# Kernel tuning notes

Hardware: AMD Instinct MI355X
Metric: run time of the kernel (lower is better)

The kernel has to match this reference:

```python
import jax, jax.numpy as jnp
import numpy as np

HEADS, DQK, DV = 4, 128, 128
HH, WW = 32, 32
SCALE = DQK ** -0.5
EPS = 1e-5


def bn(x, g, b, m, v):
    # eval-mode BatchNorm2d over channel dim of NCHW
    inv = g * jax.lax.rsqrt(v + EPS)
    return x * inv[:, None, None] + (b - m * inv)[:, None, None]


def rel_to_abs(x):
    # x: (B, Nh, L, 2L-1) -> (B, Nh, L, L)
    B, Nh, L, _ = x.shape
    x = jnp.pad(x, ((0, 0), (0, 0), (0, 0), (0, 1)))
    fx = x.reshape(B, Nh, L * 2 * L)
    fx = jnp.pad(fx, ((0, 0), (0, 0), (0, L - 1)))
    fx = fx.reshape(B, Nh, L + 1, 2 * L - 1)
    return fx[:, :, :L, L - 1:]


def rel_logits_1d(q, rel_k):
    # q: (B, Nh, H, W, D); rel_k: (2W-1, D)
    B, Nh, H, W, D = q.shape
    r = jnp.einsum('bnhwd,rd->bnhwr', q, rel_k)
    r = rel_to_abs(r.reshape(B, Nh * H, W, 2 * W - 1))
    r = r.reshape(B, Nh, H, W, W)
    return jnp.broadcast_to(r[:, :, :, None], (B, Nh, H, H, W, W))


def pos_bias(q, rel_h, rel_w):
    # q: (B, Nh, H*W, D), already scaled
    B, Nh, L, D = q.shape
    q5 = q.reshape(B, Nh, HH, WW, D)
    rw = rel_logits_1d(q5, rel_w)                     # (B,N,H,Hx,W,W)
    rw = rw.transpose(0, 1, 2, 4, 3, 5).reshape(B, Nh, HH * WW, HH * WW)
    rh = rel_logits_1d(q5.transpose(0, 1, 3, 2, 4), rel_h)  # (B,N,W,Wx,H,H)
    rh = rh.transpose(0, 1, 4, 2, 5, 3).reshape(B, Nh, HH * WW, HH * WW)
    return rw + rh


def to_heads(x):
    # (B, Nh*d, H, W) -> (B, Nh, H*W, d)
    B, C, H, W = x.shape
    x = x.reshape(B, HEADS, C // HEADS, H, W)
    return x.transpose(0, 1, 3, 4, 2).reshape(B, HEADS, H * W, C // HEADS)


def mhsa(x, w_qk, w_v, rel_h, rel_w):
    B, C, H, W = x.shape
    qk = jnp.einsum('bchw,oc->bohw', x, w_qk)
    q, k = jnp.split(qk, 2, axis=1)
    v = jnp.einsum('bchw,oc->bohw', x, w_v)
    q, k, v = to_heads(q), to_heads(k), to_heads(v)
    q = q * SCALE
    logits = jnp.einsum('bnid,bnjd->bnij', q, k) + pos_bias(q, rel_h, rel_w)
    weights = jax.nn.softmax(logits, axis=-1)
    out = jnp.einsum('bnij,bnjd->bnid', weights, v)   # (B,Nh,HW,dv)
    out = out.reshape(B, HEADS, H, W, DV).transpose(0, 1, 4, 2, 3)
    return out.reshape(B, HEADS * DV, H, W)


def setup_inputs() -> dict:
    key = jax.random.key(0)
    ks = jax.random.split(key, 12)
    d = {
        'x': jax.random.normal(ks[0], (8, 512, HH, WW), jnp.float32),
        'w_qk': jax.random.normal(ks[1], (2 * HEADS * DQK, 512), jnp.float32) * 0.02,
        'w_v': jax.random.normal(ks[2], (HEADS * DV, 512), jnp.float32) * 0.02,
        'rel_h': jax.random.normal(ks[3], (2 * HH - 1, DQK), jnp.float32) * SCALE,
        'rel_w': jax.random.normal(ks[4], (2 * WW - 1, DQK), jnp.float32) * SCALE,
        'g1': jnp.ones((512,), jnp.float32),
        'b1': jnp.zeros((512,), jnp.float32),
        'm1': jax.random.normal(ks[5], (512,), jnp.float32) * 0.1,
        'v1': jax.random.uniform(ks[6], (512,), jnp.float32) + 0.5,
        'g2': jnp.ones((512,), jnp.float32),
        'b2': jnp.zeros((512,), jnp.float32),
        'm2': jax.random.normal(ks[7], (512,), jnp.float32) * 0.1,
        'v2': jax.random.uniform(ks[8], (512,), jnp.float32) + 0.5,
        'w_fc': jax.random.normal(ks[9], (512, 512, 3, 3), jnp.float32) * 0.02,
        'bias_fc': jnp.zeros((512,), jnp.float32),
    }
    return d


def reference(x, w_qk, w_v, rel_h, rel_w, g1, b1, m1, v1, g2, b2, m2, v2, w_fc, bias_fc):
    out = jax.nn.relu(bn(x, g1, b1, m1, v1))
    out = mhsa(out, w_qk, w_v, rel_h, rel_w)
    x = out + x
    out = jax.nn.relu(bn(x, g2, b2, m2, v2))
    out = jax.lax.conv_general_dilated(
        out, w_fc, window_strides=(1, 1), padding='SAME',
        dimension_numbers=('NCHW', 'OIHW', 'NCHW')) + bias_fc[:, None, None]
    return out + x
```

## Files before the change

### kernel.cpp

```cpp
#include <hip/hip_runtime.h>

typedef __bf16 v8bf __attribute__((ext_vector_type(8)));
typedef float f32x4 __attribute__((ext_vector_type(4)));

#define DEVI static __device__ __forceinline__

DEVI v8bf load8(const __bf16* p) { return *reinterpret_cast<const v8bf*>(p); }

DEVI f32x4 mfma16(v8bf a, v8bf b, f32x4 c) {
  return __builtin_amdgcn_mfma_f32_16x16x32_bf16(a, b, c, 0, 0, 0);
}

DEVI void gld16(const __bf16* g, __bf16* l) {
  __builtin_amdgcn_global_load_lds(
      (const __attribute__((address_space(1))) unsigned int*)(const void*)g,
      (__attribute__((address_space(3))) unsigned int*)(void*)l, 16, 0, 0);
}

#define SCALE_Q 0.08838834764831845f

__global__ void k_prep(const float* __restrict__ wqk, const float* __restrict__ wv,
                       const float* __restrict__ relh, const float* __restrict__ relw,
                       const float* __restrict__ wfc, __bf16* __restrict__ wqkb,
                       __bf16* __restrict__ wvb, __bf16* __restrict__ rhb,
                       __bf16* __restrict__ rwb, __bf16* __restrict__ Wt,
                       float* __restrict__ zpad4, const float* __restrict__ x,
                       const float* __restrict__ g1, const float* __restrict__ b1,
                       const float* __restrict__ m1, const float* __restrict__ v1,
                       __bf16* __restrict__ y) {
  __shared__ float tile[32][33];
  const int bid = blockIdx.x, tid = threadIdx.x;
  if (bid >= 6472) {
    const int local = bid - 6472;
    const int b = local >> 9, c0 = ((local >> 5) & 15) * 32, s0 = (local & 31) * 32;
    const int tx = tid & 31, ty = tid >> 5;
#pragma unroll
    for (int r = 0; r < 4; ++r) {
      int c = c0 + ty + r * 8;
      float inv = g1[c] * rsqrtf(v1[c] + 1e-5f);
      float beta = b1[c] - m1[c] * inv;
      float val = x[((size_t)b * 512 + c) * 1024 + s0 + tx] * inv + beta;
      tile[ty + r * 8][tx] = fmaxf(val, 0.0f);
    }
    __syncthreads();
#pragma unroll
    for (int r = 0; r < 4; ++r) {
      int s = s0 + ty + r * 8;
      y[((size_t)b * 1024 + s) * 512 + c0 + tx] = (__bf16)tile[tx][ty + r * 8];
    }
    return;
  }
  if (bid < 2048) {
    int i = bid * 256 + tid;
    wqkb[i] = (__bf16)wqk[i];
  } else if (bid < 3072) {
    int i = (bid - 2048) * 256 + tid;
    wvb[i] = (__bf16)wv[i];
  } else if (bid < 3104) {
    int i = (bid - 3072) * 256 + tid;
    if (i < 8064) rhb[i] = (__bf16)relh[i];
  } else if (bid < 3136) {
    int i = (bid - 3104) * 256 + tid;
    if (i < 8064) rwb[i] = (__bf16)relw[i];
  } else if (bid < 4160) {
    int i = (bid - 3136) * 256 + tid;
    const float* src = wfc + (size_t)i * 9;
#pragma unroll
    for (int tap = 0; tap < 9; ++tap)
      Wt[(size_t)tap * 262144 + i] = (__bf16)src[tap];
  } else {
    int i = (bid - 4160) * 256 + tid;
    f32x4 z = {0.f, 0.f, 0.f, 0.f};
    reinterpret_cast<f32x4*>(zpad4)[i] = z;
  }
}

__global__ void k_bn2c(float* o0x2, const float* __restrict__ o1,
                       const float* __restrict__ lp, const float* __restrict__ xin,
                       const float* __restrict__ g, const float* __restrict__ bb,
                       const float* __restrict__ m, const float* __restrict__ v,
                       __bf16* __restrict__ zp) {
  __shared__ float tile[32][33];
  const int b = blockIdx.z, c0 = blockIdx.y * 32, s0 = blockIdx.x * 32;
  const int tx = threadIdx.x, ty = threadIdx.y;
  const int bnrow = b * 4 + (c0 >> 7);
  const int scol = s0 + tx;
  const float linv =
      1.0f / (lp[bnrow * 1024 + scol] + lp[32768 + bnrow * 1024 + scol]);
#pragma unroll
  for (int r = 0; r < 4; ++r) {
    int c = c0 + ty + r * 8;
    float inv = g[c] * rsqrtf(v[c] + 1e-5f);
    float beta = bb[c] - m[c] * inv;
    size_t idx = ((size_t)b * 512 + c) * 1024 + scol;
    float t = (o0x2[idx] + o1[idx]) * linv + xin[idx];
    o0x2[idx] = t;
    tile[ty + r * 8][tx] = fmaxf(t * inv + beta, 0.0f);
  }
  __syncthreads();
#pragma unroll
  for (int r = 0; r < 4; ++r) {
    int s = s0 + ty + r * 8;
    int hh = s >> 5, ww = s & 31;
    zp[(((size_t)b * 34 + hh + 1) * 34 + ww + 1) * 512 + c0 + tx] =
        (__bf16)tile[tx][ty + r * 8];
  }
}

__global__ __launch_bounds__(256) void k_proj(
    const __bf16* __restrict__ wall, const __bf16* __restrict__ y,
    __bf16* __restrict__ qout, __bf16* __restrict__ kout,
    __bf16* __restrict__ vout) {
  __shared__ __bf16 As[2][128 * 32];
  __shared__ __bf16 Bs[2][128 * 32];
  const int t = threadIdx.x;
  const int wave = t >> 6, lane = t & 63;
  const int l15 = lane & 15, quad = lane >> 4;
  const int Lb = blockIdx.x;
  const int logical = (Lb & 7) * 96 + (Lb >> 3);
  const int nt = logical / 12, mt = logical % 12;
  const int mbase = mt * 128;
  const int nbase = nt * 128;
  const int mh = (wave >> 1) * 64, nh = (wave & 1) * 64;
  const bool isv = mbase >= 1024;

  const int row0 = t >> 2, part8 = (t & 3) * 8;
  const __bf16* gA0 = wall + (size_t)(mbase + row0) * 512 + part8;
  const __bf16* gA1 = gA0 + (size_t)64 * 512;
  const __bf16* gB0 = y + (size_t)(nbase + row0) * 512 + part8;
  const __bf16* gB1 = gB0 + (size_t)64 * 512;
  const int wofs = wave * 512;

  const f32x4 fz = {0.f, 0.f, 0.f, 0.f};
  f32x4 acc[4][4];
#pragma unroll
  for (int i = 0; i < 4; ++i)
#pragma unroll
    for (int j = 0; j < 4; ++j) acc[i][j] = fz;

  gld16(gA0, &As[0][wofs]);
  gld16(gA1, &As[0][2048 + wofs]);
  gld16(gB0, &Bs[0][wofs]);
  gld16(gB1, &Bs[0][2048 + wofs]);
  __syncthreads();

#pragma unroll 1
  for (int r = 0; r < 16; ++r) {
    const int cur = r & 1;
    if (r < 15) {
      const int kn = (r + 1) * 32;
      gld16(gA0 + kn, &As[cur ^ 1][wofs]);
      gld16(gA1 + kn, &As[cur ^ 1][2048 + wofs]);
      gld16(gB0 + kn, &Bs[cur ^ 1][wofs]);
      gld16(gB1 + kn, &Bs[cur ^ 1][2048 + wofs]);
    }
    v8bf a[4], bfr[4];
#pragma unroll
    for (int i = 0; i < 4; ++i)
      a[i] = load8(&As[cur][(mh + i * 16 + l15) * 32 + quad * 8]);
#pragma unroll
    for (int j = 0; j < 4; ++j)
      bfr[j] = load8(&Bs[cur][(nh + j * 16 + l15) * 32 + quad * 8]);
    if (isv) {
#pragma unroll
      for (int i = 0; i < 4; ++i)
#pragma unroll
        for (int j = 0; j < 4; ++j) acc[i][j] = mfma16(a[i], bfr[j], acc[i][j]);
    } else {
#pragma unroll
      for (int i = 0; i < 4; ++i)
#pragma unroll
        for (int j = 0; j < 4; ++j) acc[i][j] = mfma16(bfr[j], a[i], acc[i][j]);
    }
    __syncthreads();
  }

  if (isv) {
#pragma unroll
    for (int i = 0; i < 4; ++i)
#pragma unroll
      for (int j = 0; j < 4; ++j)
#pragma unroll
        for (int r = 0; r < 4; ++r) {
          int o = mbase + mh + i * 16 + quad * 4 + r;
          int nflat = nbase + nh + j * 16 + l15;
          int b = nflat >> 10, s = nflat & 1023;
          int oe = o - 1024; int n = oe >> 7, d = oe & 127;
          vout[(((size_t)b * 4 + n) * 128 + d) * 1024 + s] = (__bf16)acc[i][j][r];
        }
  } else {
    const bool isq = mbase < 512;
#pragma unroll
    for (int i = 0; i < 4; ++i)
#pragma unroll
      for (int j = 0; j < 4; ++j)
#pragma unroll
        for (int r = 0; r < 4; ++r) {
          int o = mbase + mh + i * 16 + l15;
          int nflat = nbase + nh + j * 16 + quad * 4 + r;
          int b = nflat >> 10, s = nflat & 1023;
          float val = acc[i][j][r];
          if (isq) {
            int n = o >> 7, d = o & 127;
            qout[(((size_t)b * 4 + n) * 1024 + s) * 128 + d] = (__bf16)(val * SCALE_Q);
          } else {
            int oe = o - 512; int n = oe >> 7, d = oe & 127;
            kout[(((size_t)b * 4 + n) * 1024 + s) * 128 + d] = (__bf16)val;
          }
        }
  }
}

__global__ __launch_bounds__(256, 2) void k_attn(
    const __bf16* __restrict__ q, const __bf16* __restrict__ kmat,
    const __bf16* __restrict__ vt, const __bf16* __restrict__ relh,
    const __bf16* __restrict__ relw, float* __restrict__ o0,
    float* __restrict__ o1, float* __restrict__ lpart) {
  __shared__ __bf16 Ks[32 * 128];
  __shared__ __bf16 Vs[2][128 * 32];
  __shared__ __bf16 P[4 * 32 * 36];
  __shared__ __bf16 RWs[128][33];
  __shared__ __bf16 RHs[128][33];

  const int Lb = blockIdx.x;
  const int xcd = Lb & 7, local = Lb >> 3;
  const int bn = xcd * 4 + (local & 3);
  const int qblk = (local >> 2) & 7;
  const int half = local >> 5;
  const int s0 = qblk * 128;

  const int t = threadIdx.x;
  const int wave = t >> 6, lane = t & 63;
  const int l15 = lane & 15, quad = lane >> 4;
  const size_t hoff = ((size_t)bn) << 17;
  const int s0w = s0 + wave * 32;
  const int h0w = s0w >> 5;
  const int j00 = half * 512;

  const __bf16* kgA =
      kmat + hoff + (size_t)((t >> 2) & 31) * 128 + (t >> 7) * 32 + (t & 3) * 8;
  const __bf16* vgA = vt + hoff + (size_t)(t >> 2) * 1024 + (t & 3) * 8;
  __bf16* kswA = Ks + wave * 512;

#pragma unroll
  for (int c = 0; c < 2; ++c)
    gld16(kgA + (size_t)j00 * 128 + c * 64, kswA + c * 2048);
#pragma unroll
  for (int dh = 0; dh < 2; ++dh)
    gld16(vgA + (size_t)dh * 64 * 1024 + j00, Vs[0] + wave * 512 + dh * 2048);

  v8bf aq[2][4];
#pragma unroll
  for (int h = 0; h < 2; ++h) {
    const __bf16* qp = q + hoff + (size_t)(s0w + h * 16 + l15) * 128;
#pragma unroll
    for (int kk = 0; kk < 4; ++kk) aq[h][kk] = load8(qp + kk * 32 + quad * 8);
  }

#pragma unroll
  for (int h = 0; h < 2; ++h) {
#pragma unroll
    for (int nt = 0; nt < 4; ++nt) {
      int rr = nt * 16 + l15;
      const __bf16* bp = relw + (size_t)rr * 128;
      f32x4 acc = {0.f, 0.f, 0.f, 0.f};
#pragma unroll
      for (int kk = 0; kk < 4; ++kk)
        acc = mfma16(aq[h][kk], load8(bp + kk * 32 + quad * 8), acc);
#pragma unroll
      for (int r = 0; r < 4; ++r) {
        int row15 = quad * 4 + r;
        int wj = rr + h * 16 + row15 - 31;
        if (wj >= 0 && wj < 32)
          RWs[wave * 32 + h * 16 + row15][wj] = (__bf16)acc[r];
      }
    }
#pragma unroll
    for (int nt = 0; nt < 2; ++nt) {
      int hj = nt * 16 + l15;
      const __bf16* bp = relh + (size_t)(hj - h0w + 31) * 128;
      f32x4 acc = {0.f, 0.f, 0.f, 0.f};
#pragma unroll
      for (int kk = 0; kk < 4; ++kk)
        acc = mfma16(aq[h][kk], load8(bp + kk * 32 + quad * 8), acc);
#pragma unroll
      for (int r = 0; r < 4; ++r)
        RHs[wave * 32 + h * 16 + quad * 4 + r][hj] = (__bf16)acc[r];
    }
  }

  float rwreg[2][4][2];
#pragma unroll
  for (int h = 0; h < 2; ++h)
#pragma unroll
    for (int r = 0; r < 4; ++r) {
      const int gi = wave * 32 + h * 16 + quad * 4 + r;
      rwreg[h][r][0] = (float)RWs[gi][l15];
      rwreg[h][r][1] = (float)RWs[gi][l15 + 16];
    }

  __syncthreads();

  const f32x4 fz = {0.f, 0.f, 0.f, 0.f};
  float lsum[2][4];
#pragma unroll
  for (int h = 0; h < 2; ++h)
#pragma unroll
    for (int r = 0; r < 4; ++r) lsum[h][r] = 0.f;
  f32x4 oacc[2][8];
#pragma unroll
  for (int h = 0; h < 2; ++h)
#pragma unroll
    for (int dt = 0; dt < 8; ++dt) oacc[h][dt] = fz;
  __bf16* Pw = P + wave * 32 * 36;

#pragma unroll 1
  for (int iter = 0; iter < 16; ++iter) {
    asm volatile("s_waitcnt vmcnt(2)" ::: "memory");
    __builtin_amdgcn_s_barrier();
    __builtin_amdgcn_sched_barrier(0);

    v8bf kf[8];
#pragma unroll
    for (int nj = 0; nj < 2; ++nj)
#pragma unroll
      for (int kk = 0; kk < 4; ++kk)
        kf[nj * 4 + kk] =
            load8(&Ks[kk * 1024 + (nj * 16 + l15) * 32 + quad * 8]);

    f32x4 sacc[2][2];
    __builtin_amdgcn_s_setprio(1);
#pragma unroll
    for (int h = 0; h < 2; ++h)
#pragma unroll
      for (int nj = 0; nj < 2; ++nj) {
        f32x4 a = fz;
#pragma unroll
        for (int kk = 0; kk < 4; ++kk)
          a = mfma16(aq[h][kk], kf[nj * 4 + kk], a);
        sacc[h][nj] = a;
      }
    __builtin_amdgcn_s_setprio(0);

    const int hjb = half * 16 + iter;
#pragma unroll
    for (int h = 0; h < 2; ++h)
#pragma unroll
      for (int r = 0; r < 4; ++r) {
        const int row = h * 16 + quad * 4 + r;
        const float rh0 = (float)RHs[wave * 32 + row][hjb];
#pragma unroll
        for (int nj = 0; nj < 2; ++nj) {
          float val = sacc[h][nj][r] + rwreg[h][r][nj] + rh0;
          float p = __expf(fminf(val, 60.0f));
          lsum[h][r] += p;
          Pw[row * 36 + nj * 16 + l15] = (__bf16)p;
        }
      }
    v8bf pf[2];
#pragma unroll
    for (int h = 0; h < 2; ++h)
      pf[h] = *reinterpret_cast<const v8bf*>(&Pw[(h * 16 + l15) * 36 + quad * 8]);

    asm volatile("s_waitcnt vmcnt(0)" ::: "memory");
    __builtin_amdgcn_s_barrier();
    __builtin_amdgcn_sched_barrier(0);

    if (iter < 15) {
      const int jn = j00 + (iter + 1) * 32;
#pragma unroll
      for (int c = 0; c < 2; ++c)
        gld16(kgA + (size_t)jn * 128 + c * 64, kswA + c * 2048);
    }

    const __bf16* vcur = Vs[iter & 1];
    __builtin_amdgcn_s_setprio(1);
#pragma unroll
    for (int dt = 0; dt < 8; ++dt) {
      v8bf vf = load8(&vcur[(dt * 16 + l15) * 32 + quad * 8]);
#pragma unroll
      for (int h = 0; h < 2; ++h)
        oacc[h][dt] = mfma16(vf, pf[h], oacc[h][dt]);
    }
    __builtin_amdgcn_s_setprio(0);

    if (iter < 15) {
      __builtin_amdgcn_sched_barrier(0);
      const int jn = j00 + (iter + 1) * 32;
      __bf16* vnext = Vs[(iter + 1) & 1] + wave * 512;
#pragma unroll
      for (int dh = 0; dh < 2; ++dh)
        gld16(vgA + (size_t)dh * 64 * 1024 + jn, vnext + dh * 2048);
    }
  }

#pragma unroll
  for (int h = 0; h < 2; ++h)
#pragma unroll
    for (int r = 0; r < 4; ++r) {
#pragma unroll
      for (int msk = 8; msk >= 1; msk >>= 1)
        lsum[h][r] += __shfl_xor(lsum[h][r], msk);
    }
  if (l15 == 0) {
#pragma unroll
    for (int h = 0; h < 2; ++h)
#pragma unroll
      for (int r = 0; r < 4; ++r)
        lpart[half * 32768 + bn * 1024 + s0w + h * 16 + quad * 4 + r] =
            lsum[h][r];
  }

  {
    float* op = half ? o1 : o0;
#pragma unroll
    for (int h = 0; h < 2; ++h) {
      const int s = s0w + h * 16 + l15;
#pragma unroll
      for (int dt = 0; dt < 8; ++dt)
#pragma unroll
        for (int r = 0; r < 4; ++r) {
          int d = dt * 16 + quad * 4 + r;
          op[((size_t)bn * 128 + d) * 1024 + s] = oacc[h][dt][r];
        }
    }
  }
}

__global__ __launch_bounds__(256, 2) void k_conv(
    const __bf16* __restrict__ Wt, const __bf16* __restrict__ zp,
    float* __restrict__ part) {
  __shared__ __bf16 As[4 * 128 * 32];
  __shared__ __bf16 Bs[4 * 128 * 32];
  const int t = threadIdx.x;
  const int wave = t >> 6, lane = t & 63;
  const int l15 = lane & 15, quad = lane >> 4;

  const int Lb = blockIdx.x;
  const int logical = (Lb & 7) * 64 + (Lb >> 3);
  const int combo = logical & 7;
  const int ot = combo >> 1, sp = combo & 1;
  const int nt = logical >> 3;
  const int mbase = ot * 128;
  const int nbase = nt * 128;
  const int cs = sp * 256;
  const int mh = (wave >> 1) * 64, nh = (wave & 1) * 64;

  const int row0 = t >> 2;
  const int part8 = (t & 3) * 8;
  const __bf16* gA0 = Wt + (size_t)(mbase + row0) * 512 + cs + part8;
  const __bf16* gA1 = gA0 + (size_t)64 * 512;
  const int n0 = nbase + row0;
  const int b0 = n0 >> 10, spn = n0 & 1023;
  const __bf16* gB0 =
      zp + ((size_t)(b0 * 34 + (spn >> 5) + 1) * 34 + (spn & 31) + 1) * 512 + cs + part8;
  const __bf16* gB1 = gB0 + (size_t)2 * 34 * 512;
  const int wofs = wave * 512;

  const f32x4 fz = {0.f, 0.f, 0.f, 0.f};
  f32x4 acc[4][4];
#pragma unroll
  for (int i = 0; i < 4; ++i)
#pragma unroll
    for (int j = 0; j < 4; ++j) acc[i][j] = fz;

#pragma unroll 1
  for (int tap = 0; tap < 9; ++tap) {
    const int dh = tap / 3 - 1, dw = tap % 3 - 1;
    const size_t aoff = (size_t)tap * 512 * 512;
    const int boff = (dh * 34 + dw) * 512;
#pragma unroll 1
    for (int k0 = 0; k0 < 256; k0 += 128) {
      __syncthreads();
#pragma unroll
      for (int c = 0; c < 4; ++c) {
        const int kq = k0 + c * 32;
        gld16(gA0 + aoff + kq, As + c * 4096 + wofs);
        gld16(gA1 + aoff + kq, As + c * 4096 + 2048 + wofs);
        gld16(gB0 + boff + kq, Bs + c * 4096 + wofs);
        gld16(gB1 + boff + kq, Bs + c * 4096 + 2048 + wofs);
      }
      __syncthreads();
#pragma unroll
      for (int c = 0; c < 4; ++c) {
        v8bf a[4], bfr[4];
#pragma unroll
        for (int i = 0; i < 4; ++i)
          a[i] = load8(&As[c * 4096 + (mh + i * 16 + l15) * 32 + quad * 8]);
#pragma unroll
        for (int j = 0; j < 4; ++j)
          bfr[j] = load8(&Bs[c * 4096 + (nh + j * 16 + l15) * 32 + quad * 8]);
#pragma unroll
        for (int i = 0; i < 4; ++i)
#pragma unroll
          for (int j = 0; j < 4; ++j) acc[i][j] = mfma16(a[i], bfr[j], acc[i][j]);
      }
    }
  }

  float* pout = part + (size_t)sp * 8 * 512 * 1024;
#pragma unroll
  for (int i = 0; i < 4; ++i)
#pragma unroll
    for (int j = 0; j < 4; ++j)
#pragma unroll
      for (int r = 0; r < 4; ++r) {
        int o = mbase + mh + i * 16 + quad * 4 + r;
        int nn = nbase + nh + j * 16 + l15;
        int bb2 = nn >> 10, s = nn & 1023;
        pout[((size_t)bb2 * 512 + o) * 1024 + s] = acc[i][j][r];
      }
}

__global__ void k_sum(const float* __restrict__ part, const float* __restrict__ bias,
                      const float* __restrict__ x2, float* __restrict__ out) {
  int i = blockIdx.x * 256 + threadIdx.x;
  int o = (i >> 8) & 511;
  f32x4 p0 = reinterpret_cast<const f32x4*>(part)[i];
  f32x4 p1 = reinterpret_cast<const f32x4*>(part + (size_t)8 * 512 * 1024)[i];
  f32x4 xr = reinterpret_cast<const f32x4*>(x2)[i];
  float bo = bias[o];
  f32x4 r;
#pragma unroll
  for (int c = 0; c < 4; ++c) r[c] = p0[c] + p1[c] + bo + xr[c];
  reinterpret_cast<f32x4*>(out)[i] = r;
}

extern "C" void kernel_launch(void* const* d_in, const int* in_sizes, int n_in,
                              void* d_out, int out_size, void* d_ws, size_t ws_size,
                              hipStream_t stream) {
  const float* x    = (const float*)d_in[0];
  const float* wqk  = (const float*)d_in[1];
  const float* wv   = (const float*)d_in[2];
  const float* relh = (const float*)d_in[3];
  const float* relw = (const float*)d_in[4];
  const float* g1   = (const float*)d_in[5];
  const float* b1   = (const float*)d_in[6];
  const float* m1   = (const float*)d_in[7];
  const float* v1   = (const float*)d_in[8];
  const float* g2   = (const float*)d_in[9];
  const float* b2   = (const float*)d_in[10];
  const float* m2   = (const float*)d_in[11];
  const float* v2   = (const float*)d_in[12];
  const float* wfc  = (const float*)d_in[13];
  const float* bfc  = (const float*)d_in[14];
  float* out = (float*)d_out;

  char* p = (char*)d_ws;
  __bf16* y    = (__bf16*)p; p += (size_t)8 * 1024 * 512 * 2;
  __bf16* qb   = (__bf16*)p; p += (size_t)8 * 4 * 1024 * 128 * 2;
  __bf16* kb   = (__bf16*)p; p += (size_t)8 * 4 * 1024 * 128 * 2;
  __bf16* vb   = (__bf16*)p; p += (size_t)8 * 4 * 1024 * 128 * 2;
  __bf16* Wt   = (__bf16*)p; p += (size_t)9 * 512 * 512 * 2;
  __bf16* wqkb = (__bf16*)p; p += (size_t)1024 * 512 * 2;
  __bf16* wvb  = (__bf16*)p; p += (size_t)512 * 512 * 2;
  __bf16* rhb  = (__bf16*)p; p += 32768;
  __bf16* rwb  = (__bf16*)p; p += 32768;
  float*  x2   = (float*)p;  p += (size_t)8 * 512 * 1024 * 4;
  __bf16* zpad = (__bf16*)p; p += (size_t)8 * 34 * 34 * 512 * 2;
  float* lpart = (float*)d_ws;
  float* o0 = x2;
  float* o1 = (float*)d_out;
  float* part = (float*)d_ws;

  k_prep<<<dim3(10568), dim3(256), 0, stream>>>(wqk, wv, relh, relw, wfc,
                                                wqkb, wvb, rhb, rwb, Wt,
                                                (float*)zpad, x, g1, b1, m1, v1, y);
  k_proj<<<dim3(768), dim3(256), 0, stream>>>(wqkb, y, qb, kb, vb);
  k_attn<<<dim3(512), dim3(256), 0, stream>>>(qb, kb, vb, rhb, rwb, o0, o1, lpart);
  k_bn2c<<<dim3(32, 16, 8), dim3(32, 8), 0, stream>>>(o0, o1, lpart, x,
                                                      g2, b2, m2, v2, zpad);
  k_conv<<<dim3(512), dim3(256), 0, stream>>>(Wt, zpad, part);
  k_sum<<<dim3(4096), dim3(256), 0, stream>>>(part, bfc, x2, out);
}
```

Measured before the change: 237.5 us.

## Process 64 keys per attention iteration instead of 32

The attention loop now handles two 32-key sub-tiles per iteration. This halves the number of iterations, barriers and waitcnt stalls, and stages double-sized K and V tiles in shared memory. The relative-height bias table is cut to the 16 columns this block's half actually uses, which saves LDS and MFMA work in the prologue. The trade is more shared memory (larger K, V and P buffers) and more registers for the wider score and P fragments, which may reduce occupancy under the 2-blocks-per-CU launch bound.

```diff
diff --git a/kernel.cpp b/kernel.cpp
--- a/kernel.cpp
+++ b/kernel.cpp
@@ -216,11 +216,11 @@
     const __bf16* __restrict__ vt, const __bf16* __restrict__ relh,
     const __bf16* __restrict__ relw, float* __restrict__ o0,
     float* __restrict__ o1, float* __restrict__ lpart) {
-  __shared__ __bf16 Ks[32 * 128];
-  __shared__ __bf16 Vs[2][128 * 32];
-  __shared__ __bf16 P[4 * 32 * 36];
+  __shared__ __bf16 Ks[2 * 4096];
+  __shared__ __bf16 Vs[2][2 * 4096];
+  __shared__ __bf16 P[4 * 32 * 72];
   __shared__ __bf16 RWs[128][33];
-  __shared__ __bf16 RHs[128][33];
+  __shared__ __bf16 RHs[128][17];
 
   const int Lb = blockIdx.x;
   const int xcd = Lb & 7, local = Lb >> 3;
@@ -240,14 +240,20 @@
   const __bf16* kgA =
       kmat + hoff + (size_t)((t >> 2) & 31) * 128 + (t >> 7) * 32 + (t & 3) * 8;
   const __bf16* vgA = vt + hoff + (size_t)(t >> 2) * 1024 + (t & 3) * 8;
-  __bf16* kswA = Ks + wave * 512;
-
-#pragma unroll
-  for (int c = 0; c < 2; ++c)
-    gld16(kgA + (size_t)j00 * 128 + c * 64, kswA + c * 2048);
-#pragma unroll
-  for (int dh = 0; dh < 2; ++dh)
-    gld16(vgA + (size_t)dh * 64 * 1024 + j00, Vs[0] + wave * 512 + dh * 2048);
+  const int wofs = wave * 512;
+
+#pragma unroll
+  for (int jh = 0; jh < 2; ++jh)
+#pragma unroll
+    for (int c = 0; c < 2; ++c)
+      gld16(kgA + (size_t)(j00 + jh * 32) * 128 + c * 64,
+            Ks + jh * 4096 + wofs + c * 2048);
+#pragma unroll
+  for (int jh = 0; jh < 2; ++jh)
+#pragma unroll
+    for (int dh = 0; dh < 2; ++dh)
+      gld16(vgA + (size_t)dh * 64 * 1024 + j00 + jh * 32,
+            Vs[0] + jh * 4096 + wofs + dh * 2048);
 
   v8bf aq[2][4];
 #pragma unroll
@@ -257,13 +263,14 @@
     for (int kk = 0; kk < 4; ++kk) aq[h][kk] = load8(qp + kk * 32 + quad * 8);
   }
 
+  const f32x4 fz = {0.f, 0.f, 0.f, 0.f};
 #pragma unroll
   for (int h = 0; h < 2; ++h) {
 #pragma unroll
     for (int nt = 0; nt < 4; ++nt) {
       int rr = nt * 16 + l15;
       const __bf16* bp = relw + (size_t)rr * 128;
-      f32x4 acc = {0.f, 0.f, 0.f, 0.f};
+      f32x4 acc = fz;
 #pragma unroll
       for (int kk = 0; kk < 4; ++kk)
         acc = mfma16(aq[h][kk], load8(bp + kk * 32 + quad * 8), acc);
@@ -275,17 +282,16 @@
           RWs[wave * 32 + h * 16 + row15][wj] = (__bf16)acc[r];
       }
     }
-#pragma unroll
-    for (int nt = 0; nt < 2; ++nt) {
-      int hj = nt * 16 + l15;
+    {
+      int hj = half * 16 + l15;
       const __bf16* bp = relh + (size_t)(hj - h0w + 31) * 128;
-      f32x4 acc = {0.f, 0.f, 0.f, 0.f};
+      f32x4 acc = fz;
 #pragma unroll
       for (int kk = 0; kk < 4; ++kk)
         acc = mfma16(aq[h][kk], load8(bp + kk * 32 + quad * 8), acc);
 #pragma unroll
       for (int r = 0; r < 4; ++r)
-        RHs[wave * 32 + h * 16 + quad * 4 + r][hj] = (__bf16)acc[r];
+        RHs[wave * 32 + h * 16 + quad * 4 + r][l15] = (__bf16)acc[r];
     }
   }
 
@@ -301,7 +307,6 @@
 
   __syncthreads();
 
-  const f32x4 fz = {0.f, 0.f, 0.f, 0.f};
   float lsum[2][4];
 #pragma unroll
   for (int h = 0; h < 2; ++h)
@@ -312,85 +317,102 @@
   for (int h = 0; h < 2; ++h)
 #pragma unroll
     for (int dt = 0; dt < 8; ++dt) oacc[h][dt] = fz;
-  __bf16* Pw = P + wave * 32 * 36;
+  __bf16* Pw = P + wave * 32 * 72;
 
 #pragma unroll 1
-  for (int iter = 0; iter < 16; ++iter) {
-    asm volatile("s_waitcnt vmcnt(2)" ::: "memory");
+  for (int iter = 0; iter < 8; ++iter) {
+    asm volatile("s_waitcnt vmcnt(4)" ::: "memory");
     __builtin_amdgcn_s_barrier();
     __builtin_amdgcn_sched_barrier(0);
 
-    v8bf kf[8];
-#pragma unroll
-    for (int nj = 0; nj < 2; ++nj)
-#pragma unroll
-      for (int kk = 0; kk < 4; ++kk)
-        kf[nj * 4 + kk] =
-            load8(&Ks[kk * 1024 + (nj * 16 + l15) * 32 + quad * 8]);
-
-    f32x4 sacc[2][2];
+    f32x4 sacc[2][4];
     __builtin_amdgcn_s_setprio(1);
 #pragma unroll
-    for (int h = 0; h < 2; ++h)
-#pragma unroll
-      for (int nj = 0; nj < 2; ++nj) {
-        f32x4 a = fz;
+    for (int njh = 0; njh < 2; ++njh) {
+      v8bf kf[8];
+#pragma unroll
+      for (int nj1 = 0; nj1 < 2; ++nj1)
 #pragma unroll
         for (int kk = 0; kk < 4; ++kk)
-          a = mfma16(aq[h][kk], kf[nj * 4 + kk], a);
-        sacc[h][nj] = a;
-      }
+          kf[nj1 * 4 + kk] = load8(
+              &Ks[njh * 4096 + kk * 1024 + (nj1 * 16 + l15) * 32 + quad * 8]);
+#pragma unroll
+      for (int h = 0; h < 2; ++h)
+#pragma unroll
+        for (int nj1 = 0; nj1 < 2; ++nj1) {
+          f32x4 a = fz;
+#pragma unroll
+          for (int kk = 0; kk < 4; ++kk)
+            a = mfma16(aq[h][kk], kf[nj1 * 4 + kk], a);
+          sacc[h][njh * 2 + nj1] = a;
+        }
+    }
     __builtin_amdgcn_s_setprio(0);
 
-    const int hjb = half * 16 + iter;
+    const int hjr = iter * 2;
 #pragma unroll
     for (int h = 0; h < 2; ++h)
 #pragma unroll
       for (int r = 0; r < 4; ++r) {
         const int row = h * 16 + quad * 4 + r;
-        const float rh0 = (float)RHs[wave * 32 + row][hjb];
-#pragma unroll
-        for (int nj = 0; nj < 2; ++nj) {
-          float val = sacc[h][nj][r] + rwreg[h][r][nj] + rh0;
+        const float rh0 = (float)RHs[wave * 32 + row][hjr];
+        const float rh1 = (float)RHs[wave * 32 + row][hjr + 1];
+#pragma unroll
+        for (int nj = 0; nj < 4; ++nj) {
+          float val = sacc[h][nj][r] + rwreg[h][r][nj & 1] + ((nj & 2) ? rh1 : rh0);
           float p = __expf(fminf(val, 60.0f));
           lsum[h][r] += p;
-          Pw[row * 36 + nj * 16 + l15] = (__bf16)p;
+          Pw[row * 72 + (nj >> 1) * 36 + (nj & 1) * 16 + l15] = (__bf16)p;
         }
       }
-    v8bf pf[2];
+    v8bf pf[2][2];
 #pragma unroll
     for (int h = 0; h < 2; ++h)
-      pf[h] = *reinterpret_cast<const v8bf*>(&Pw[(h * 16 + l15) * 36 + quad * 8]);
+#pragma unroll
+      for (int kk2 = 0; kk2 < 2; ++kk2)
+        pf[h][kk2] = *reinterpret_cast<const v8bf*>(
+            &Pw[(h * 16 + l15) * 72 + kk2 * 36 + quad * 8]);
 
     asm volatile("s_waitcnt vmcnt(0)" ::: "memory");
     __builtin_amdgcn_s_barrier();
     __builtin_amdgcn_sched_barrier(0);
 
-    if (iter < 15) {
-      const int jn = j00 + (iter + 1) * 32;
-#pragma unroll
-      for (int c = 0; c < 2; ++c)
-        gld16(kgA + (size_t)jn * 128 + c * 64, kswA + c * 2048);
+    if (iter < 7) {
+      const int jn = j00 + (iter + 1) * 64;
+#pragma unroll
+      for (int jh = 0; jh < 2; ++jh)
+#pragma unroll
+        for (int c = 0; c < 2; ++c)
+          gld16(kgA + (size_t)(jn + jh * 32) * 128 + c * 64,
+                Ks + jh * 4096 + wofs + c * 2048);
     }
 
     const __bf16* vcur = Vs[iter & 1];
     __builtin_amdgcn_s_setprio(1);
 #pragma unroll
     for (int dt = 0; dt < 8; ++dt) {
-      v8bf vf = load8(&vcur[(dt * 16 + l15) * 32 + quad * 8]);
-#pragma unroll
-      for (int h = 0; h < 2; ++h)
-        oacc[h][dt] = mfma16(vf, pf[h], oacc[h][dt]);
+      f32x4 a0 = oacc[0][dt], a1 = oacc[1][dt];
+#pragma unroll
+      for (int kk2 = 0; kk2 < 2; ++kk2) {
+        v8bf vf = load8(&vcur[kk2 * 4096 + (dt * 16 + l15) * 32 + quad * 8]);
+        a0 = mfma16(vf, pf[0][kk2], a0);
+        a1 = mfma16(vf, pf[1][kk2], a1);
+      }
+      oacc[0][dt] = a0;
+      oacc[1][dt] = a1;
     }
     __builtin_amdgcn_s_setprio(0);
 
-    if (iter < 15) {
+    if (iter < 7) {
       __builtin_amdgcn_sched_barrier(0);
-      const int jn = j00 + (iter + 1) * 32;
-      __bf16* vnext = Vs[(iter + 1) & 1] + wave * 512;
-#pragma unroll
-      for (int dh = 0; dh < 2; ++dh)
-        gld16(vgA + (size_t)dh * 64 * 1024 + jn, vnext + dh * 2048);
+      const int jn = j00 + (iter + 1) * 64;
+      __bf16* vnext = Vs[(iter + 1) & 1];
+#pragma unroll
+      for (int jh = 0; jh < 2; ++jh)
+#pragma unroll
+        for (int dh = 0; dh < 2; ++dh)
+          gld16(vgA + (size_t)dh * 64 * 1024 + jn + jh * 32,
+                vnext + jh * 4096 + wofs + dh * 2048);
     }
   }
 
```

After: 234.3 us, median of 2. About the same (-1.3%).
